# Kernel optimization log

Hardware: AMD Instinct MI355X
Metric: run time of the kernel (lower is better)

Reference implementation:

```python
import jax, jax.numpy as jnp
import numpy as np

B = 8192
EPS = 1e-5  # BatchNorm eps (torch default)


def binarize(x):
    # sign binarization with straight-through estimator (matches the .data trick
    # in BinarizeConv2d/BinarizeLinear: forward sees +-1, backward sees identity)
    s = jnp.where(x >= 0, 1.0, -1.0).astype(x.dtype)
    return x + jax.lax.stop_gradient(s - x)


def conv2d(x, w, stride, pad):
    return jax.lax.conv_general_dilated(
        x, w, window_strides=stride, padding=pad,
        dimension_numbers=('NCHW', 'OIHW', 'NCHW'))


def bn(x, g, b, m, v):
    # eval-mode BatchNorm2d folded into one scale+shift per channel
    inv = g * jax.lax.rsqrt(v + EPS)
    return x * inv[None, :, None, None] + (b - m * inv)[None, :, None, None]


def maxpool_w2(x):
    # MaxPool2d(kernel=(1,2), stride=(1,2))
    return jax.lax.reduce_window(x, -jnp.inf, jax.lax.max,
                                 (1, 1, 1, 2), (1, 1, 1, 2), 'VALID')


def setup_inputs() -> dict:
    key = jax.random.key(0)
    ks = jax.random.split(key, 32)
    d = {}
    d['x'] = jax.random.normal(ks[0], (B, 1, 6, 128), jnp.float32)

    def w(k, shape):
        return jax.random.normal(k, shape, jnp.float32) * 0.05

    # conv weights (OIHW) and biases
    d['w1'] = w(ks[1], (32, 1, 1, 9));    d['b1'] = w(ks[2], (32,))
    d['w2'] = w(ks[3], (64, 32, 1, 3));   d['b2'] = w(ks[4], (64,))
    d['w3'] = w(ks[5], (128, 64, 1, 3));  d['b3'] = w(ks[6], (128,))
    d['w4'] = w(ks[7], (128, 128, 6, 1)); d['b4'] = w(ks[8], (128,))
    # BatchNorm params (gamma, beta, running_mean, running_var)
    for i, c in zip((1, 2, 3, 4), (32, 64, 128, 128)):
        kk = jax.random.split(ks[8 + i], 4)
        d[f'g{i}'] = 1.0 + 0.1 * jax.random.normal(kk[0], (c,), jnp.float32)
        d[f'be{i}'] = 0.1 * jax.random.normal(kk[1], (c,), jnp.float32)
        d[f'm{i}'] = 0.1 * jax.random.normal(kk[2], (c,), jnp.float32)
        d[f'v{i}'] = jax.random.uniform(kk[3], (c,), jnp.float32, 0.5, 1.5)
    # fc: BinarizeLinear(2048, 10)
    d['wf'] = w(ks[20], (10, 2048))
    d['bf'] = w(ks[21], (10,))
    return d


def reference(x, w1, b1, w2, b2, w3, b3, w4, b4,
              g1, be1, m1, v1, g2, be2, m2, v2,
              g3, be3, m3, v3, g4, be4, m4, v4, wf, bf):
    # block 1: first layer keeps real-valued input, binarized weights
    h = conv2d(x, binarize(w1), (1, 2), [(0, 0), (4, 4)]) + b1[None, :, None, None]
    h = jnp.clip(bn(h, g1, be1, m1, v1), -1.0, 1.0)   # Hardtanh
    h = maxpool_w2(h)                                  # [B,32,6,32]
    # block 2: binarized activations + weights
    h = conv2d(binarize(h), binarize(w2), (1, 1), [(0, 0), (1, 1)]) + b2[None, :, None, None]
    h = jnp.clip(bn(h, g2, be2, m2, v2), -1.0, 1.0)    # [B,64,6,32]
    # block 3
    h = conv2d(binarize(h), binarize(w3), (1, 1), [(0, 0), (1, 1)]) + b3[None, :, None, None]
    h = jnp.clip(bn(h, g3, be3, m3, v3), -1.0, 1.0)
    h = maxpool_w2(h)                                  # [B,128,6,16]
    # block 4: (6,1) kernel collapses H
    h = conv2d(binarize(h), binarize(w4), (1, 1), [(0, 0), (0, 0)]) + b4[None, :, None, None]
    h = jnp.clip(bn(h, g4, be4, m4, v4), -1.0, 1.0)    # [B,128,1,16]
    h = h.reshape(h.shape[0], -1)                      # [B,2048]
    return binarize(h) @ binarize(wf).T + bf           # [B,10]
```

## Files before the change

### kernel.cpp

```cpp
#include <hip/hip_runtime.h>
#include <cstdint>
#include <cstddef>

#define BN_EPS 1e-5f
#define BATCH 8192

typedef unsigned long long u64;
typedef uint32_t u32;
typedef int v4i __attribute__((ext_vector_type(4)));
typedef int v16i __attribute__((ext_vector_type(16)));

__device__ __forceinline__ u32 f2k(float f) {
    u32 u = __float_as_uint(f);
    return (u >> 31) ? ~u : (u | 0x80000000u);
}
__device__ __forceinline__ float k2f(u32 k) {
    u32 u = (k & 0x80000000u) ? (k ^ 0x80000000u) : ~k;
    return __uint_as_float(u);
}
__device__ __forceinline__ float bn_eval(float conv, float B, float iv, float sh) {
    return __fadd_rn(__fmul_rn(__fadd_rn(conv, B), iv), sh);
}

__global__ __launch_bounds__(256) void prep_all(
    const float* w1, const float* b1, const float* w2, const float* b2,
    const float* w3, const float* b3, const float* w4, const float* b4,
    const float* wf,
    const float* g1, const float* be1, const float* m1, const float* v1,
    const float* g2, const float* be2, const float* m2, const float* v2,
    const float* g3, const float* be3, const float* m3, const float* v3,
    const float* g4, const float* be4, const float* m4, const float* v4,
    float* s1f, float* T1, u32* wt2w, int* T2,
    uint4* b3i8, int* C3, u64* wt4, int* T4, u64* wtf) {
    int t = blockIdx.x * 256 + threadIdx.x;

    if (t < 384) {
        int co = t / 12, k = t % 12;
        float val = 0.f;
        if (k < 9) {
            float iv = g1[co] * rsqrtf(v1[co] + BN_EPS);
            float d = (iv < 0.f) ? -1.f : 1.f;
            val = ((w1[co * 9 + k] >= 0.f) ? 1.f : -1.f) * d;
        }
        s1f[t] = val;
    } else if (t < 416) {
        int co = t - 384;
        float iv = g1[co] * rsqrtf(v1[co] + BN_EPS);
        float sh = be1[co] - m1[co] * iv;
        float B = b1[co];
        bool flip = (iv < 0.f);
        auto pred = [&](float sp) {
            float sum = flip ? -sp : sp;
            return bn_eval(sum, B, iv, sh) >= 0.f;
        };
        u32 lo = f2k(-3.0e38f), hi = f2k(3.0e38f);
        float Tv;
        if (pred(k2f(lo))) Tv = k2f(lo);
        else if (!pred(k2f(hi))) Tv = __uint_as_float(0x7F800000u);
        else {
            while (hi - lo > 1u) {
                u32 mid = lo + ((hi - lo) >> 1);
                if (pred(k2f(mid))) hi = mid; else lo = mid;
            }
            Tv = k2f(hi);
        }
        T1[co] = Tv;
    } else if (t < 608) {
        int idx = t - 416;
        int co = idx / 3, kw = idx % 3;
        float iv = g2[co] * rsqrtf(v2[co] + BN_EPS);
        bool flip = (iv < 0.f);
        u32 wb = 0;
        for (int ci = 0; ci < 32; ++ci)
            wb |= (u32)((w2[(co * 32 + ci) * 3 + kw] >= 0.f) != flip) << ci;
        wt2w[co * 4 + kw] = wb;
    } else if (t < 800) {
        int idx = t - 608;
        int co = idx & 63, cls = idx >> 6;
        float iv = g2[co] * rsqrtf(v2[co] + BN_EPS);
        float sh = be2[co] - m2[co] * iv;
        float B = b2[co];
        bool flip = (iv < 0.f);
        int spur = 0, nv = 3;
        if (cls == 1) { nv = 2; for (int ci = 0; ci < 32; ++ci) spur += (int)((w2[(co * 32 + ci) * 3 + 0] >= 0.f) != flip); }
        if (cls == 2) { nv = 2; for (int ci = 0; ci < 32; ++ci) spur += (int)((w2[(co * 32 + ci) * 3 + 2] >= 0.f) != flip); }
        int maxp = 32 * nv + spur;
        int T = -1;
        for (int p = 0; p <= maxp; ++p) {
            int conv = flip ? (2 * (p - spur) - 32 * nv) : (32 * nv - 2 * (p - spur));
            float y = bn_eval((float)conv, B, iv, sh);
            if ((y >= 0.f) && (T == p - 1)) T = p;
        }
        T2[cls * 64 + co] = T;
    } else if (t < 2336) {
        int idx = t - 800;
        int q = idx >> 7, n = idx & 127;
        float iv = g3[n] * rsqrtf(v3[n] + BN_EPS);
        bool flip = (iv < 0.f);
        int kw = q >> 2, ci0 = (q & 3) * 16;
        u32 wd[4] = {0, 0, 0, 0};
        for (int j = 0; j < 16; ++j) {
            int ci = ci0 + j;
            bool pos = (w3[(n * 64 + ci) * 3 + kw] >= 0.f) != flip;
            u32 byte = pos ? 0x01u : 0xFFu;
            wd[j >> 2] |= byte << (8 * (j & 3));
        }
        b3i8[idx] = make_uint4(wd[0], wd[1], wd[2], wd[3]);
    } else if (t < 2464) {
        int co = t - 2336;
        float iv = g3[co] * rsqrtf(v3[co] + BN_EPS);
        float sh = be3[co] - m3[co] * iv;
        float B = b3[co];
        int C = 1000;
        if (iv >= 0.f) {
            for (int v = -192; v <= 192; v += 2)
                if (bn_eval((float)v, B, iv, sh) >= 0.f) { C = v; break; }
        } else {
            for (int v = 192; v >= -192; v -= 2)
                if (bn_eval((float)v, B, iv, sh) >= 0.f) { C = -v; break; }
        }
        C3[co] = C;
    } else if (t < 4000) {
        int idx = t - 2464;
        int j = idx & 1, ch = idx >> 1;
        int co = ch / 6, h = ch % 6;
        float iv = g4[co] * rsqrtf(v4[co] + BN_EPS);
        bool flip = (iv < 0.f);
        u64 wb = 0;
        for (int cb = 0; cb < 64; ++cb) {
            int ci = j * 64 + cb;
            wb |= (u64)((w4[(co * 128 + ci) * 6 + h] >= 0.f) != flip) << cb;
        }
        wt4[idx] = wb;
    } else if (t < 4128) {
        int co = t - 4000;
        float iv = g4[co] * rsqrtf(v4[co] + BN_EPS);
        float sh = be4[co] - m4[co] * iv;
        float B = b4[co];
        bool flip = (iv < 0.f);
        int T = -1;
        for (int p = 0; p <= 768; ++p) {
            int conv = flip ? (2 * p - 768) : (768 - 2 * p);
            float y = bn_eval((float)conv, B, iv, sh);
            if ((y >= 0.f) && (T == p - 1)) T = p;
        }
        T4[co] = T;
    } else if (t < 4448) {
        int idx = t - 4128;
        int o = idx / 32, wi = idx % 32;
        u64 wb = 0;
        for (int fb = 0; fb < 64; ++fb)
            wb |= (u64)(wf[o * 2048 + wi * 64 + fb] >= 0.f) << fb;
        wtf[idx] = wb;
    }
}

#define RB 24
__global__ __launch_bounds__(256, 3) void mega123_kernel(
    const float* __restrict__ x, const float4* __restrict__ s1p, const float* __restrict__ T1g,
    const uint4* __restrict__ wt2v, const int* __restrict__ T2g,
    const uint4* __restrict__ b3i8, const int* __restrict__ C3g,
    u32* __restrict__ a3u32) {
    __shared__ uint4 sB3[1536];
    __shared__ u64 sLUT[256];
    __shared__ short sC3[128];
    __shared__ uint4 sW2[64];
    __shared__ short sT2[192];
    __shared__ float sX[8][140];
    __shared__ u32 sA1[8][32];
    __shared__ u64 sA2[RB][32];
    int t = threadIdx.x;
    for (int i = t; i < 1536; i += 256) sB3[i] = b3i8[i];
    {
        u32 b = t & 255;
        u64 e = 0;
#pragma unroll
        for (int j = 0; j < 8; ++j)
            e |= (((b >> j) & 1) ? 0x01ull : 0xFFull) << (8 * j);
        if (t < 256) sLUT[t] = e;
    }
    if (t < 128) sC3[t] = (short)C3g[t];
    if (t < 64) sW2[t] = wt2v[t];
    if (t < 192) sT2[t] = (short)T2g[t];

    int co = t & 31, lane = t & 63;
    float4 wa = s1p[co * 3 + 0];
    float4 wb = s1p[co * 3 + 1];
    float wc = s1p[co * 3 + 2].x;
    float Tt = T1g[co];

    int bh0 = blockIdx.x * RB;
    for (int ch = 0; ch < 3; ++ch) {
        __syncthreads();
        for (int i = t; i < 8 * 140; i += 256) {
            int r = i / 140, c = i % 140;
            float v = 0.f;
            if (c >= 4 && c < 132) v = x[(size_t)(bh0 + ch * 8 + r) * 128 + (c - 4)];
            sX[r][c] = v;
        }
        __syncthreads();
        {
            int rr = t >> 5;
            const float* xr = sX[rr];
            float4 A0 = *(const float4*)&xr[0];
            float4 A1 = *(const float4*)&xr[4];
            float4 A2 = *(const float4*)&xr[8];
            u32 myword = 0;
#pragma unroll
            for (int wp = 0; wp < 32; ++wp) {
                float sum0 = 0.f, sum1 = 0.f;
                sum0 = fmaf(wa.x, A0.x, sum0);  sum1 = fmaf(wa.x, A0.z, sum1);
                sum0 = fmaf(wa.y, A0.y, sum0);  sum1 = fmaf(wa.y, A0.w, sum1);
                sum0 = fmaf(wa.z, A0.z, sum0);  sum1 = fmaf(wa.z, A1.x, sum1);
                sum0 = fmaf(wa.w, A0.w, sum0);  sum1 = fmaf(wa.w, A1.y, sum1);
                sum0 = fmaf(wb.x, A1.x, sum0);  sum1 = fmaf(wb.x, A1.z, sum1);
                sum0 = fmaf(wb.y, A1.y, sum0);  sum1 = fmaf(wb.y, A1.w, sum1);
                sum0 = fmaf(wb.z, A1.z, sum0);  sum1 = fmaf(wb.z, A2.x, sum1);
                sum0 = fmaf(wb.w, A1.w, sum0);  sum1 = fmaf(wb.w, A2.y, sum1);
                sum0 = fmaf(wc,   A2.x, sum0);  sum1 = fmaf(wc,   A2.z, sum1);
                bool pred = fmaxf(sum0, sum1) >= Tt;
                u64 mk = __ballot(pred);
                u32 hw = (lane < 32) ? (u32)mk : (u32)(mk >> 32);
                if ((lane & 31) == wp) myword = hw;
                A0 = A1; A1 = A2;
                A2 = *(const float4*)&xr[4 * wp + 12];
            }
            sA1[((t >> 6) << 1) + (lane >> 5)][lane & 31] = myword;
        }
        __syncthreads();
        {
            int r = t >> 5, wp = t & 31;
            u32 am = sA1[r][wp];
            u32 al = (wp > 0) ? sA1[r][wp - 1] : 0u;
            u32 ar = (wp < 31) ? sA1[r][wp + 1] : 0u;
            const short* Tp = &sT2[(wp == 0) ? 64 : ((wp == 31) ? 128 : 0)];
            u64 word2 = 0;
#pragma unroll
            for (int c = 0; c < 64; ++c) {
                uint4 w2v = sW2[c];
                int p = __popc(al ^ w2v.x) + __popc(am ^ w2v.y) + __popc(ar ^ w2v.z);
                word2 |= (u64)(p <= (int)Tp[c]) << c;
            }
            sA2[ch * 8 + r][wp] = word2;
        }
    }
    __syncthreads();

    int wq = t >> 6, m = lane & 31, half = lane >> 5;
    const int prTab[8] = {0, 1, 4, 5, 8, 9, 12, 13};
    for (int r6 = 0; r6 < 6; ++r6) {
        int row = wq * 6 + r6;
        u64 aw = sA2[row][m];
        u64 wm1 = (m > 0) ? sA2[row][m - 1] : 0ull;
        u64 wp1 = (m < 31) ? sA2[row][m + 1] : 0ull;

        v4i A[6];
#pragma unroll
        for (int kk = 0; kk < 6; ++kk) {
            const int kw = kk >> 1;
            u64 word = (kw == 0) ? wm1 : ((kw == 1) ? aw : wp1);
            bool valid = !((kw == 0 && m == 0) || (kw == 2 && m == 31));
            int ci0 = ((kk & 1) << 5) + (half << 4);
            u32 bits = (u32)(word >> ci0) & 0xFFFFu;
            u64 lo = sLUT[bits & 0xFF];
            u64 hi = sLUT[bits >> 8];
            if (!valid) { lo = 0; hi = 0; }
            union { u64 q[2]; v4i v; } u;
            u.q[0] = lo; u.q[1] = hi;
            A[kk] = u.v;
        }
        u32 outv = 0;
#pragma unroll
        for (int nt = 0; nt < 4; ++nt) {
            v16i acc;
#pragma unroll
            for (int i = 0; i < 16; ++i) acc[i] = 0;
#pragma unroll
            for (int kk = 0; kk < 6; ++kk) {
                int q = kk * 2 + half;
                union { uint4 u4; v4i v; } bu;
                bu.u4 = sB3[q * 128 + nt * 32 + m];
                acc = __builtin_amdgcn_mfma_i32_32x32x32_i8(A[kk], bu.v, acc, 0, 0, 0);
            }
            int tc = (int)sC3[nt * 32 + m];
#pragma unroll
            for (int rp = 0; rp < 8; ++rp) {
                bool c = (acc[2 * rp] >= tc) || (acc[2 * rp + 1] >= tc);
                u64 mk = __ballot(c);
                int LA = (nt << 4) | prTab[rp];
                int LB = LA + 2;
                outv = (lane == LA) ? (u32)mk : outv;
                outv = (lane == LB) ? (u32)(mk >> 32) : outv;
            }
        }
        a3u32[(size_t)(bh0 + row) * 64 + ((lane & 15) << 2) + (lane >> 4)] = outv;
    }
}

__global__ __launch_bounds__(256) void layer4_fc_kernel(
    const u64* __restrict__ a3, const u64* __restrict__ wt4, const int* __restrict__ T4,
    const u64* __restrict__ wtf, const float* __restrict__ bf, float* __restrict__ out) {
    __shared__ u64 sW4[1536];
    __shared__ u64 sWf[320];
    __shared__ u64 sFeat[16][32];
    __shared__ int sT[128];
    __shared__ float sBf[10];
    int t = threadIdx.x;
    {
        ulonglong2* d = (ulonglong2*)sW4;
        const ulonglong2* s = (const ulonglong2*)wt4;
        for (int i = t; i < 768; i += 256) d[i] = s[i];
        ulonglong2* df = (ulonglong2*)sWf;
        const ulonglong2* sf = (const ulonglong2*)wtf;
        if (t < 160) df[t] = sf[t];
    }
    if (t < 128) sT[t] = T4[t];
    if (t < 10) sBf[t] = bf[t];
    __syncthreads();
    int bb = t >> 4, w = t & 15, lane = t & 63, g = lane >> 4;
    int b = blockIdx.x * 16 + bb;
    u64 av[12];
#pragma unroll
    for (int h = 0; h < 6; ++h) {
        av[h * 2 + 0] = a3[(size_t)b * 192 + h * 32 + w * 2 + 0];
        av[h * 2 + 1] = a3[(size_t)b * 192 + h * 32 + w * 2 + 1];
    }
    u64 acc = 0;
#pragma unroll 8
    for (int c = 0; c < 128; ++c) {
        const u64* wr = &sW4[c * 12];
        int p = 0;
#pragma unroll
        for (int q = 0; q < 12; ++q) p += __popcll(av[q] ^ wr[q]);
        u64 mk = __ballot(p <= sT[c]);
        u64 field = (mk >> (g * 16)) & 0xFFFFull;
        acc |= field << ((c & 3) << 4);
        if ((c & 3) == 3) {
            if (w == 0) sFeat[bb][c >> 2] = acc;
            acc = 0;
        }
    }
    __syncthreads();
    if (t < 160) {
        int fb = t / 10, o = t % 10;
        int p = 0;
#pragma unroll
        for (int wi = 0; wi < 32; ++wi) p += __popcll(sFeat[fb][wi] ^ sWf[o * 32 + wi]);
        out[(size_t)(blockIdx.x * 16 + fb) * 10 + o] = __fadd_rn((float)(2048 - 2 * p), sBf[o]);
    }
}

extern "C" void kernel_launch(void* const* d_in, const int* in_sizes, int n_in,
                              void* d_out, int out_size, void* d_ws, size_t ws_size,
                              hipStream_t stream) {
    const float* x  = (const float*)d_in[0];
    const float* w1 = (const float*)d_in[1];  const float* b1 = (const float*)d_in[2];
    const float* w2 = (const float*)d_in[3];  const float* b2 = (const float*)d_in[4];
    const float* w3 = (const float*)d_in[5];  const float* b3 = (const float*)d_in[6];
    const float* w4 = (const float*)d_in[7];  const float* b4 = (const float*)d_in[8];
    const float* g1 = (const float*)d_in[9];  const float* be1 = (const float*)d_in[10];
    const float* m1 = (const float*)d_in[11]; const float* v1 = (const float*)d_in[12];
    const float* g2 = (const float*)d_in[13]; const float* be2 = (const float*)d_in[14];
    const float* m2 = (const float*)d_in[15]; const float* v2 = (const float*)d_in[16];
    const float* g3 = (const float*)d_in[17]; const float* be3 = (const float*)d_in[18];
    const float* m3 = (const float*)d_in[19]; const float* v3 = (const float*)d_in[20];
    const float* g4 = (const float*)d_in[21]; const float* be4 = (const float*)d_in[22];
    const float* m4 = (const float*)d_in[23]; const float* v4 = (const float*)d_in[24];
    const float* wf = (const float*)d_in[25]; const float* bf = (const float*)d_in[26];
    float* out = (float*)d_out;

    char* ws = (char*)d_ws;
    u64* a3 = (u64*)(ws + 0);
    const size_t S = 12582912;
    uint4* b3i8 = (uint4*)(ws + S + 0);
    u64*  wt4  = (u64*) (ws + S + 24576);
    u64*  wtf  = (u64*) (ws + S + 36864);
    u32*  wt2w = (u32*) (ws + S + 39424);
    float* s1f = (float*)(ws + S + 40448);
    float* T1  = (float*)(ws + S + 41984);
    int*  T2   = (int*)  (ws + S + 42112);
    int*  C3   = (int*)  (ws + S + 42880);
    int*  T4   = (int*)  (ws + S + 43392);

    prep_all<<<18, 256, 0, stream>>>(w1, b1, w2, b2, w3, b3, w4, b4, wf,
                                     g1, be1, m1, v1, g2, be2, m2, v2,
                                     g3, be3, m3, v3, g4, be4, m4, v4,
                                     s1f, T1, wt2w, T2, b3i8, C3, wt4, T4, wtf);

    mega123_kernel<<<(BATCH * 6) / RB, 256, 0, stream>>>(
        x, (const float4*)s1f, T1, (const uint4*)wt2w, T2, b3i8, C3, (u32*)a3);
    layer4_fc_kernel<<<BATCH / 16, 256, 0, stream>>>(a3, wt4, T4, wtf, bf, out);
}
```

Baseline: 270.3 us.

## Fuse layer4 and FC into the layers 1-3 mega kernel via shared memory

Merges the layer4+FC kernel into the main kernel so that each block of 24 rows (4 batch items) computes its a3 activations into shared memory and then runs layer 4 and the final linear layer directly. This removes the 12.5MB global round-trip of a3 and one kernel launch. The shared memory is manually aliased across phases and the weight tables for layer 4 and the FC layer are reloaded per block. The FC stage now uses only 40 threads per block.

```diff
diff --git a/kernel.cpp b/kernel.cpp
--- a/kernel.cpp
+++ b/kernel.cpp
@@ -156,19 +156,30 @@
 }
 
 #define RB 24
-__global__ __launch_bounds__(256, 3) void mega123_kernel(
+__global__ __launch_bounds__(256, 3) void mega_kernel(
     const float* __restrict__ x, const float4* __restrict__ s1p, const float* __restrict__ T1g,
     const uint4* __restrict__ wt2v, const int* __restrict__ T2g,
     const uint4* __restrict__ b3i8, const int* __restrict__ C3g,
-    u32* __restrict__ a3u32) {
-    __shared__ uint4 sB3[1536];
-    __shared__ u64 sLUT[256];
-    __shared__ short sC3[128];
-    __shared__ uint4 sW2[64];
-    __shared__ short sT2[192];
-    __shared__ float sX[8][140];
-    __shared__ u32 sA1[8][32];
-    __shared__ u64 sA2[RB][32];
+    const u64* __restrict__ wt4, const int* __restrict__ T4g,
+    const u64* __restrict__ wtf, const float* __restrict__ bfg,
+    float* __restrict__ out) {
+    __shared__ __attribute__((aligned(16))) char smem[40576];
+    uint4* sB3 = (uint4*)smem;
+    u64*  sLUT = (u64*)(smem + 24576);
+    short* sC3 = (short*)(smem + 26624);
+    uint4* sW2 = (uint4*)(smem + 26880);
+    short* sT2 = (short*)(smem + 27904);
+    float* sX  = (float*)(smem + 28288);
+    u32*  sA1  = (u32*)(smem + 32768);
+    u64*  sA2  = (u64*)(smem + 34432);
+    u64*  sW4  = (u64*)smem;
+    u64*  sWf  = (u64*)(smem + 12288);
+    u64*  sFeat = (u64*)(smem + 26880);
+    short* sT4 = (short*)(smem + 27904);
+    float* sBf = (float*)(smem + 28160);
+    u32*  sA3u = (u32*)(smem + 28288);
+    u64*  sA3q = (u64*)(smem + 28288);
+
     int t = threadIdx.x;
     for (int i = t; i < 1536; i += 256) sB3[i] = b3i8[i];
     {
@@ -196,12 +207,12 @@
             int r = i / 140, c = i % 140;
             float v = 0.f;
             if (c >= 4 && c < 132) v = x[(size_t)(bh0 + ch * 8 + r) * 128 + (c - 4)];
-            sX[r][c] = v;
+            sX[r * 140 + c] = v;
         }
         __syncthreads();
         {
             int rr = t >> 5;
-            const float* xr = sX[rr];
+            const float* xr = &sX[rr * 140];
             float4 A0 = *(const float4*)&xr[0];
             float4 A1 = *(const float4*)&xr[4];
             float4 A2 = *(const float4*)&xr[8];
@@ -225,14 +236,14 @@
                 A0 = A1; A1 = A2;
                 A2 = *(const float4*)&xr[4 * wp + 12];
             }
-            sA1[((t >> 6) << 1) + (lane >> 5)][lane & 31] = myword;
+            sA1[(((t >> 6) << 1) + (lane >> 5)) * 32 + (lane & 31)] = myword;
         }
         __syncthreads();
         {
             int r = t >> 5, wp = t & 31;
-            u32 am = sA1[r][wp];
-            u32 al = (wp > 0) ? sA1[r][wp - 1] : 0u;
-            u32 ar = (wp < 31) ? sA1[r][wp + 1] : 0u;
+            u32 am = sA1[r * 32 + wp];
+            u32 al = (wp > 0) ? sA1[r * 32 + wp - 1] : 0u;
+            u32 ar = (wp < 31) ? sA1[r * 32 + wp + 1] : 0u;
             const short* Tp = &sT2[(wp == 0) ? 64 : ((wp == 31) ? 128 : 0)];
             u64 word2 = 0;
 #pragma unroll
@@ -241,7 +252,7 @@
                 int p = __popc(al ^ w2v.x) + __popc(am ^ w2v.y) + __popc(ar ^ w2v.z);
                 word2 |= (u64)(p <= (int)Tp[c]) << c;
             }
-            sA2[ch * 8 + r][wp] = word2;
+            sA2[(ch * 8 + r) * 32 + wp] = word2;
         }
     }
     __syncthreads();
@@ -250,9 +261,9 @@
     const int prTab[8] = {0, 1, 4, 5, 8, 9, 12, 13};
     for (int r6 = 0; r6 < 6; ++r6) {
         int row = wq * 6 + r6;
-        u64 aw = sA2[row][m];
-        u64 wm1 = (m > 0) ? sA2[row][m - 1] : 0ull;
-        u64 wp1 = (m < 31) ? sA2[row][m + 1] : 0ull;
+        u64 aw = sA2[row * 32 + m];
+        u64 wm1 = (m > 0) ? sA2[row * 32 + m - 1] : 0ull;
+        u64 wp1 = (m < 31) ? sA2[row * 32 + m + 1] : 0ull;
 
         v4i A[6];
 #pragma unroll
@@ -293,60 +304,50 @@
                 outv = (lane == LB) ? (u32)(mk >> 32) : outv;
             }
         }
-        a3u32[(size_t)(bh0 + row) * 64 + ((lane & 15) << 2) + (lane >> 4)] = outv;
-    }
-}
-
-__global__ __launch_bounds__(256) void layer4_fc_kernel(
-    const u64* __restrict__ a3, const u64* __restrict__ wt4, const int* __restrict__ T4,
-    const u64* __restrict__ wtf, const float* __restrict__ bf, float* __restrict__ out) {
-    __shared__ u64 sW4[1536];
-    __shared__ u64 sWf[320];
-    __shared__ u64 sFeat[16][32];
-    __shared__ int sT[128];
-    __shared__ float sBf[10];
-    int t = threadIdx.x;
+        sA3u[row * 64 + ((lane & 15) << 2) + (lane >> 4)] = outv;
+    }
+    __syncthreads();
+
+    for (int i = t; i < 1536; i += 256) sW4[i] = wt4[i];
+    for (int i = t; i < 320; i += 256) sWf[i] = wtf[i];
+    if (t < 128) sT4[t] = (short)T4g[t];
+    if (t < 10) sBf[t] = bfg[t];
+    __syncthreads();
+
     {
-        ulonglong2* d = (ulonglong2*)sW4;
-        const ulonglong2* s = (const ulonglong2*)wt4;
-        for (int i = t; i < 768; i += 256) d[i] = s[i];
-        ulonglong2* df = (ulonglong2*)sWf;
-        const ulonglong2* sf = (const ulonglong2*)wtf;
-        if (t < 160) df[t] = sf[t];
-    }
-    if (t < 128) sT[t] = T4[t];
-    if (t < 10) sBf[t] = bf[t];
+        int bb = t >> 6;
+        int w = lane & 15;
+        int cg = lane >> 4;
+        u64 av[12];
+#pragma unroll
+        for (int h = 0; h < 6; ++h) {
+            av[h * 2 + 0] = sA3q[(bb * 6 + h) * 32 + w * 2 + 0];
+            av[h * 2 + 1] = sA3q[(bb * 6 + h) * 32 + w * 2 + 1];
+        }
+        u64 acc = 0;
+#pragma unroll 4
+        for (int c = 0; c < 32; ++c) {
+            int cc = cg * 32 + c;
+            const u64* wr = &sW4[cc * 12];
+            int p = 0;
+#pragma unroll
+            for (int q = 0; q < 12; ++q) p += __popcll(av[q] ^ wr[q]);
+            u64 mk = __ballot(p <= (int)sT4[cc]);
+            u64 field = (mk >> (cg * 16)) & 0xFFFFull;
+            acc |= field << ((c & 3) << 4);
+            if ((c & 3) == 3) {
+                if (w == (c >> 2)) sFeat[bb * 32 + cg * 8 + (c >> 2)] = acc;
+                acc = 0;
+            }
+        }
+    }
     __syncthreads();
-    int bb = t >> 4, w = t & 15, lane = t & 63, g = lane >> 4;
-    int b = blockIdx.x * 16 + bb;
-    u64 av[12];
-#pragma unroll
-    for (int h = 0; h < 6; ++h) {
-        av[h * 2 + 0] = a3[(size_t)b * 192 + h * 32 + w * 2 + 0];
-        av[h * 2 + 1] = a3[(size_t)b * 192 + h * 32 + w * 2 + 1];
-    }
-    u64 acc = 0;
-#pragma unroll 8
-    for (int c = 0; c < 128; ++c) {
-        const u64* wr = &sW4[c * 12];
-        int p = 0;
-#pragma unroll
-        for (int q = 0; q < 12; ++q) p += __popcll(av[q] ^ wr[q]);
-        u64 mk = __ballot(p <= sT[c]);
-        u64 field = (mk >> (g * 16)) & 0xFFFFull;
-        acc |= field << ((c & 3) << 4);
-        if ((c & 3) == 3) {
-            if (w == 0) sFeat[bb][c >> 2] = acc;
-            acc = 0;
-        }
-    }
-    __syncthreads();
-    if (t < 160) {
+    if (t < 40) {
         int fb = t / 10, o = t % 10;
         int p = 0;
 #pragma unroll
-        for (int wi = 0; wi < 32; ++wi) p += __popcll(sFeat[fb][wi] ^ sWf[o * 32 + wi]);
-        out[(size_t)(blockIdx.x * 16 + fb) * 10 + o] = __fadd_rn((float)(2048 - 2 * p), sBf[o]);
+        for (int wi = 0; wi < 32; ++wi) p += __popcll(sFeat[fb * 32 + wi] ^ sWf[o * 32 + wi]);
+        out[(size_t)(blockIdx.x * 4 + fb) * 10 + o] = __fadd_rn((float)(2048 - 2 * p), sBf[o]);
     }
 }
 
@@ -370,8 +371,7 @@
     float* out = (float*)d_out;
 
     char* ws = (char*)d_ws;
-    u64* a3 = (u64*)(ws + 0);
-    const size_t S = 12582912;
+    const size_t S = 0;
     uint4* b3i8 = (uint4*)(ws + S + 0);
     u64*  wt4  = (u64*) (ws + S + 24576);
     u64*  wtf  = (u64*) (ws + S + 36864);
@@ -387,7 +387,7 @@
                                      g3, be3, m3, v3, g4, be4, m4, v4,
                                      s1f, T1, wt2w, T2, b3i8, C3, wt4, T4, wtf);
 
-    mega123_kernel<<<(BATCH * 6) / RB, 256, 0, stream>>>(
-        x, (const float4*)s1f, T1, (const uint4*)wt2w, T2, b3i8, C3, (u32*)a3);
-    layer4_fc_kernel<<<BATCH / 16, 256, 0, stream>>>(a3, wt4, T4, wtf, bf, out);
-}
+    mega_kernel<<<(BATCH * 6) / RB, 256, 0, stream>>>(
+        x, (const float4*)s1f, T1, (const uint4*)wt2w, T2, b3i8, C3,
+        wt4, T4, wtf, bf, out);
+}
```

Result: faster. 256.5 us (-5.1%).
